# Performance work log

Measured on AMD Instinct MI355X. Metric: run time of the kernel, lower is better.

Reference implementation:

```python
import jax, jax.numpy as jnp
import numpy as np
import math

B, N, M = 4, 8192, 4096
POINT_DIM = 3
TIME_EMBED_DIM = 128
HIDDEN = (128, 256, 512, 512, 256)
EPS = 1e-5


def _silu(x):
    return x * jax.nn.sigmoid(x)


def _ln(x, g, b):
    m = x.mean(-1, keepdims=True)
    v = ((x - m) ** 2).mean(-1, keepdims=True)
    return (x - m) / jnp.sqrt(v + EPS) * g + b


def _blk(x, w, b, g, be):
    return _silu(_ln(x @ w + b, g, be))


def _linear_params(key, din, dout):
    return jax.random.normal(key, (din, dout), jnp.float32) * 0.02, jnp.zeros((dout,), jnp.float32)


def setup_inputs() -> dict:
    key = jax.random.key(0)
    ks = jax.random.split(key, 16)
    inp = {
        "noisy_points": jax.random.normal(ks[0], (B, N, POINT_DIM), jnp.float32),
        "target_points": jax.random.normal(ks[1], (B, M, POINT_DIM), jnp.float32),
        "timesteps": jax.random.uniform(ks[2], (B,), jnp.float32) * 1000.0,
    }
    # time embedding MLP: 128 -> 512 -> 512
    inp["te_w1"], inp["te_b1"] = _linear_params(ks[3], TIME_EMBED_DIM, TIME_EMBED_DIM * 4)
    inp["te_w2"], inp["te_b2"] = _linear_params(ks[4], TIME_EMBED_DIM * 4, TIME_EMBED_DIM * 4)
    # encoders: 6->128, 128->256, 256->512 (each Linear + LayerNorm)
    enc_dims = [(POINT_DIM * 2, HIDDEN[0]), (HIDDEN[0], HIDDEN[1]), (HIDDEN[1], HIDDEN[2])]
    for i, (di, do) in enumerate(enc_dims):
        inp[f"enc_w{i}"], inp[f"enc_b{i}"] = _linear_params(ks[5 + i], di, do)
        inp[f"enc_g{i}"] = jnp.ones((do,), jnp.float32)
        inp[f"enc_be{i}"] = jnp.zeros((do,), jnp.float32)
    # middle: (512 + 512) -> 512
    mid = HIDDEN[2]
    inp["mid_w"], inp["mid_b"] = _linear_params(ks[8], mid + TIME_EMBED_DIM * 4, mid)
    inp["mid_g"] = jnp.ones((mid,), jnp.float32)
    inp["mid_be"] = jnp.zeros((mid,), jnp.float32)
    # decoders: (512+256)->512, (512+128)->256
    dec_dims = [(mid + HIDDEN[1], HIDDEN[3]), (mid + HIDDEN[0], HIDDEN[4])]
    for i, (di, do) in enumerate(dec_dims):
        inp[f"dec_w{i}"], inp[f"dec_b{i}"] = _linear_params(ks[9 + i], di, do)
        inp[f"dec_g{i}"] = jnp.ones((do,), jnp.float32)
        inp[f"dec_be{i}"] = jnp.zeros((do,), jnp.float32)
    # output proj: 256 -> 3
    inp["out_w"], inp["out_b"] = _linear_params(ks[11], HIDDEN[4], POINT_DIM)
    return inp


def _time_embedding(timesteps, te_w1, te_b1, te_w2, te_b2):
    half = TIME_EMBED_DIM // 2
    freqs = jnp.exp(jnp.arange(half, dtype=jnp.float32) * (-math.log(10000.0) / (half - 1)))
    emb = timesteps[:, None] * freqs[None, :]  # (B, half)
    emb = jnp.concatenate([jnp.sin(emb), jnp.cos(emb)], axis=-1)  # (B, 128)
    return _silu(emb @ te_w1 + te_b1) @ te_w2 + te_b2  # (B, 512)


def _forward(noisy_points, target_points, timesteps,
             te_w1, te_b1, te_w2, te_b2,
             enc_w0, enc_b0, enc_g0, enc_be0,
             enc_w1, enc_b1, enc_g1, enc_be1,
             enc_w2, enc_b2, enc_g2, enc_be2,
             mid_w, mid_b, mid_g, mid_be,
             dec_w0, dec_b0, dec_g0, dec_be0,
             dec_w1, dec_b1, dec_g1, dec_be1,
             out_w, out_b):
    # nearest-neighbor lookup: squared distances share argmin with cdist
    d2 = (jnp.sum(noisy_points ** 2, -1)[:, :, None]
          + jnp.sum(target_points ** 2, -1)[:, None, :]
          - 2.0 * jnp.einsum('bnd,bmd->bnm', noisy_points, target_points))  # (B,N,M)
    idx = jnp.argmin(d2, axis=-1)  # (B,N)
    nearest = jnp.take_along_axis(
        target_points, jnp.broadcast_to(idx[:, :, None], idx.shape + (POINT_DIM,)), axis=1)
    x = jnp.concatenate([noisy_points, nearest], axis=-1)  # (B,N,6)
    skip0 = _blk(x, enc_w0, enc_b0, enc_g0, enc_be0)        # (B,N,128)
    skip1 = _blk(skip0, enc_w1, enc_b1, enc_g1, enc_be1)    # (B,N,256)
    x = _blk(skip1, enc_w2, enc_b2, enc_g2, enc_be2)        # (B,N,512)
    temb = _time_embedding(timesteps, te_w1, te_b1, te_w2, te_b2)  # (B,512)
    tfeat = jnp.broadcast_to(temb[:, None, :], (x.shape[0], x.shape[1], temb.shape[-1]))
    x = _blk(jnp.concatenate([x, tfeat], -1), mid_w, mid_b, mid_g, mid_be)      # (B,N,512)
    x = _blk(jnp.concatenate([x, skip1], -1), dec_w0, dec_b0, dec_g0, dec_be0)  # (B,N,512)
    x = _blk(jnp.concatenate([x, skip0], -1), dec_w1, dec_b1, dec_g1, dec_be1)  # (B,N,256)
    return x @ out_w + out_b  # (B,N,3)


def reference(noisy_points, target_points, timesteps,
              te_w1, te_b1, te_w2, te_b2,
              enc_w0, enc_b0, enc_g0, enc_be0,
              enc_w1, enc_b1, enc_g1, enc_be1,
              enc_w2, enc_b2, enc_g2, enc_be2,
              mid_w, mid_b, mid_g, mid_be,
              dec_w0, dec_b0, dec_g0, dec_be0,
              dec_w1, dec_b1, dec_g1, dec_be1,
              out_w, out_b):
    return _forward(noisy_points, target_points, timesteps,
                    te_w1, te_b1, te_w2, te_b2,
                    enc_w0, enc_b0, enc_g0, enc_be0,
                    enc_w1, enc_b1, enc_g1, enc_be1,
                    enc_w2, enc_b2, enc_g2, enc_be2,
                    mid_w, mid_b, mid_g, mid_be,
                    dec_w0, dec_b0, dec_g0, dec_be0,
                    dec_w1, dec_b1, dec_g1, dec_be1,
                    out_w, out_b)
```

## Files before the change

### kernel.cpp

```cpp
#include <hip/hip_runtime.h>
#include <stdint.h>

#define RTOT 32768
#define CR   16384
#define NPTS 8192
#define MPTS 4096
#define NCH 8
#define CHM 512

typedef float f4v __attribute__((ext_vector_type(4)));
typedef short s8v __attribute__((ext_vector_type(8)));

__device__ __forceinline__ float bq(float f) {
    union { float f; uint32_t i; } u; u.f = f;
    u.i = (u.i + 0x7FFFu + ((u.i >> 16) & 1u)) & 0xFFFF0000u;
    return u.f;
}
__device__ __forceinline__ unsigned short f2bfu(float f) {
    union { float f; uint32_t i; } u; u.f = f;
    return (unsigned short)((u.i + 0x7FFFu + ((u.i >> 16) & 1u)) >> 16);
}
__device__ __forceinline__ float bfu2f(unsigned short s) {
    union { uint32_t i; float f; } u; u.i = ((uint32_t)s) << 16;
    return u.f;
}

__global__ __launch_bounds__(256) void transpose_split_kernel(
    const float* __restrict__ W, unsigned short* __restrict__ Wth,
    unsigned short* __restrict__ Wtl, int K, int N) {
    int i = blockIdx.x * 256 + threadIdx.x;
    if (i < K * N) {
        int n = i / K;
        int k = i % K;
        float w = W[(size_t)k * N + n];
        unsigned short h = f2bfu(w);
        Wth[i] = h;
        Wtl[i] = f2bfu(w - bfu2f(h));
    }
}

__global__ __launch_bounds__(256) void te0_dual(
    const float* __restrict__ ts,
    const float* __restrict__ w1, const float* __restrict__ b1,
    float* __restrict__ e1, float* __restrict__ e1q) {
    const bool Qv = (blockIdx.z == 1);
    __shared__ float emb[128];
    const int b = blockIdx.y;
    const int j = blockIdx.x * 256 + threadIdx.x;
    float t = ts[b];
    if (threadIdx.x < 128) {
        int k = threadIdx.x & 63;
        float f = expf((float)k * -0.14619587892025688f);
        float a = t * f;
        float v = (threadIdx.x < 64) ? sinf(a) : cosf(a);
        emb[threadIdx.x] = Qv ? bq(v) : v;
    }
    __syncthreads();
    float acc = 0.f;
    #pragma unroll 8
    for (int k = 0; k < 128; k++) {
        float w = w1[(size_t)k * 512 + j];
        acc += emb[k] * (Qv ? bq(w) : w);
    }
    acc += b1[j];
    if (Qv) {
        float h = bq(acc);
        float sg = bq(1.f / (1.f + expf(-h)));
        e1q[b * 512 + j] = bq(h * sg);
    } else {
        e1[b * 512 + j] = acc / (1.f + expf(-acc));
    }
}

__global__ __launch_bounds__(256) void te1_dual(
    const float* __restrict__ e1, const float* __restrict__ e1q,
    const float* __restrict__ w2, const float* __restrict__ b2,
    unsigned short* __restrict__ tembh, unsigned short* __restrict__ tembl,
    unsigned short* __restrict__ tembq) {
    const bool Qv = (blockIdx.z == 1);
    __shared__ float es[512];
    const int b = blockIdx.y;
    const int j = blockIdx.x * 256 + threadIdx.x;
    const float* src = Qv ? e1q : e1;
    float v0 = src[b * 512 + threadIdx.x];
    float v1 = src[b * 512 + 256 + threadIdx.x];
    es[threadIdx.x] = Qv ? bq(v0) : v0;
    es[256 + threadIdx.x] = Qv ? bq(v1) : v1;
    __syncthreads();
    float acc = 0.f;
    #pragma unroll 8
    for (int k = 0; k < 512; k++) {
        float w = w2[(size_t)k * 512 + j];
        acc += es[k] * (Qv ? bq(w) : w);
    }
    acc += b2[j];
    if (Qv) {
        tembq[b * 512 + j] = f2bfu(acc);
    } else {
        unsigned short h = f2bfu(acc);
        tembh[b * 512 + j] = h;
        tembl[b * 512 + j] = f2bfu(acc - bfu2f(h));
    }
}

__global__ __launch_bounds__(256) void nn_partial_kernel(
    const float* __restrict__ NP, const float* __restrict__ TP,
    double* __restrict__ pd, int* __restrict__ pi) {
    __shared__ float tx[CHM], ty[CHM], tz[CHM];
    __shared__ double t264[CHM];
    const int t = threadIdx.x;
    const int r = blockIdx.x * 256 + t;
    const int b = r >> 13;
    const int ch = blockIdx.y;
    const int m0 = ch * CHM;
    for (int i = t; i < CHM; i += 256) {
        const float* p = TP + ((size_t)b * MPTS + m0 + i) * 3;
        float x = p[0], y = p[1], z = p[2];
        tx[i] = x; ty[i] = y; tz[i] = z;
        t264[i] = (double)x * x + (double)y * y + (double)z * z;
    }
    __syncthreads();
    const float* q = NP + (size_t)r * 3;
    double nx = (double)q[0], ny = (double)q[1], nz = (double)q[2];
    double sn = nx * nx + ny * ny + nz * nz;
    double g1 = 1e300; int j1 = 0;
    for (int m = 0; m < CHM; m++) {
        double d = (sn + t264[m]) - 2.0 * (nx * tx[m] + ny * ty[m] + nz * tz[m]);
        if (d < g1) { g1 = d; j1 = m; }
    }
    size_t o = (size_t)r * NCH + ch;
    pd[o] = g1;
    pi[o] = m0 + j1;
}

__global__ __launch_bounds__(256) void nn_merge_kernel(
    const float* __restrict__ NP, const float* __restrict__ TP,
    const double* __restrict__ pd, const int* __restrict__ pi,
    float* __restrict__ X0) {
    const int r = blockIdx.x * 256 + threadIdx.x;
    double g1 = 1e300; int j1 = 0;
    #pragma unroll
    for (int c = 0; c < NCH; c++) {
        size_t o = (size_t)r * NCH + c;
        double d = pd[o]; int i = pi[o];
        if (d < g1) { g1 = d; j1 = i; }
    }
    const int b = r >> 13;
    const float* tp = TP + ((size_t)b * MPTS + j1) * 3;
    const float* q = NP + (size_t)r * 3;
    float* o = X0 + (size_t)r * 6;
    o[0] = q[0]; o[1] = q[1]; o[2] = q[2];
    o[3] = tp[0]; o[4] = tp[1]; o[5] = tp[2];
}

__global__ __launch_bounds__(256) void layer0_dual(
    const float* __restrict__ X0, const float* __restrict__ W0,
    const float* __restrict__ b0, const float* __restrict__ g0,
    const float* __restrict__ e0,
    unsigned short* __restrict__ OutQ,
    unsigned short* __restrict__ OutFh, unsigned short* __restrict__ OutFl) {
    const bool Qp = (blockIdx.y == 0);
    const int wave = threadIdx.x >> 6;
    const int lane = threadIdx.x & 63;
    const int r = blockIdx.x * 4 + wave;
    float xk[6];
    #pragma unroll
    for (int k = 0; k < 6; k++) {
        float v = X0[(size_t)r * 6 + k];
        xk[k] = Qp ? bq(v) : v;
    }
    const int j0 = lane, j1 = lane + 64;
    float y0 = 0.f, y1 = 0.f;
    #pragma unroll
    for (int k = 0; k < 6; k++) {
        float w0 = W0[k * 128 + j0], w1 = W0[k * 128 + j1];
        y0 += xk[k] * (Qp ? bq(w0) : w0);
        y1 += xk[k] * (Qp ? bq(w1) : w1);
    }
    y0 += b0[j0];
    y1 += b0[j1];
    if (Qp) { y0 = bq(y0); y1 = bq(y1); }
    float s = y0 + y1;
    #pragma unroll
    for (int m = 1; m < 64; m <<= 1) s += __shfl_xor(s, m, 64);
    float mean = s * (1.f / 128.f);
    if (Qp) {
        mean = bq(mean);
        float c0 = bq(y0 - mean), c1 = bq(y1 - mean);
        float q0 = bq(c0 * c0), q1 = bq(c1 * c1);
        float sv = q0 + q1;
        #pragma unroll
        for (int m = 1; m < 64; m <<= 1) sv += __shfl_xor(sv, m, 64);
        float var = bq(sv * (1.f / 128.f));
        float sd = bq(sqrtf(bq(var + 1e-5f)));
        float d0 = bq(c0 / sd), d1 = bq(c1 / sd);
        d0 = bq(bq(d0 * g0[j0]) + e0[j0]);
        d1 = bq(bq(d1 * g0[j1]) + e0[j1]);
        float s0 = bq(1.f / (1.f + expf(-d0)));
        float s1 = bq(1.f / (1.f + expf(-d1)));
        OutQ[(size_t)r * 128 + j0] = f2bfu(d0 * s0);
        OutQ[(size_t)r * 128 + j1] = f2bfu(d1 * s1);
    } else {
        float sq = y0 * y0 + y1 * y1;
        #pragma unroll
        for (int m = 1; m < 64; m <<= 1) sq += __shfl_xor(sq, m, 64);
        float var = sq * (1.f / 128.f) - mean * mean;
        float rstd = rsqrtf(var + 1e-5f);
        float n0 = (y0 - mean) * rstd * g0[j0] + e0[j0];
        float n1 = (y1 - mean) * rstd * g0[j1] + e0[j1];
        float v0 = n0 / (1.f + expf(-n0));
        float v1 = n1 / (1.f + expf(-n1));
        unsigned short h0 = f2bfu(v0), h1 = f2bfu(v1);
        OutFh[(size_t)r * 128 + j0] = h0;
        OutFl[(size_t)r * 128 + j0] = f2bfu(v0 - bfu2f(h0));
        OutFh[(size_t)r * 128 + j1] = h1;
        OutFl[(size_t)r * 128 + j1] = f2bfu(v1 - bfu2f(h1));
    }
}

#define AP 72

template <int NOUT, bool FP>
__device__ __forceinline__ void mfma_body(
    const unsigned short* __restrict__ A1a, const unsigned short* __restrict__ A1b, int K1,
    const unsigned short* __restrict__ A2a, const unsigned short* __restrict__ A2b, int K2, int shift,
    const unsigned short* __restrict__ Wth,
    const unsigned short* __restrict__ Wtl,
    const float* __restrict__ bias,
    const float* __restrict__ gamma,
    const float* __restrict__ beta,
    unsigned short* __restrict__ OutQ,
    unsigned short* __restrict__ OutFh, unsigned short* __restrict__ OutFl,
    float* __restrict__ OutF32, int K,
    unsigned short* AhB, unsigned short* AlB, float (*lnS)[16], float (*lnQ)[16]) {
    constexpr int BNW = NOUT / 4;
    constexpr int CT = BNW / 16;
    constexpr int CHK = FP ? 2 : 4;

    const int tid = threadIdx.x;
    const int wave = tid >> 6;
    const int lane = tid & 63;
    const int q = lane >> 4;
    const int c = lane & 15;
    const int r0 = blockIdx.x * 64;
    const int trow = tid >> 2;
    const int tcol = (tid & 3) << 4;
    const int r = r0 + trow;

    f4v acc[4][CT];
    #pragma unroll
    for (int rt = 0; rt < 4; rt++)
        #pragma unroll
        for (int ct = 0; ct < CT; ct++)
            acc[rt][ct] = (f4v)0.f;

    s8v qa[2], qb[2];
    auto loadA = [&](int k0) {
        const int kk = k0 + tcol;
        const unsigned short *sa, *sb;
        size_t idx;
        if (k0 < K1) { sa = A1a; sb = A1b; idx = (size_t)r * K1 + kk; }
        else         { sa = A2a; sb = A2b; idx = (size_t)(r >> shift) * K2 + (kk - K1); }
        qa[0] = *(const s8v*)(sa + idx);
        qa[1] = *(const s8v*)(sa + idx + 8);
        if (FP) {
            qb[0] = *(const s8v*)(sb + idx);
            qb[1] = *(const s8v*)(sb + idx + 8);
        }
    };

    loadA(0);
    int cur = 0;
    for (int k0 = 0; k0 < K; k0 += 64) {
        unsigned short* Ah = AhB + cur * (64 * AP);
        unsigned short* Al = AlB + cur * (64 * AP);
        *(s8v*)(&Ah[trow * AP + tcol]) = qa[0];
        *(s8v*)(&Ah[trow * AP + tcol + 8]) = qa[1];
        if (FP) {
            *(s8v*)(&Al[trow * AP + tcol]) = qb[0];
            *(s8v*)(&Al[trow * AP + tcol + 8]) = qb[1];
        }
        if (k0 + 64 < K) loadA(k0 + 64);
        __syncthreads();
        __builtin_amdgcn_s_setprio(1);
        #pragma unroll
        for (int kh = 0; kh < 2; kh++) {
            const int kb = k0 + kh * 32;
            #pragma unroll
            for (int ctb = 0; ctb < CT; ctb += CHK) {
                s8v bh[CHK], bl[CHK];
                #pragma unroll
                for (int j = 0; j < CHK; j++) {
                    int col = wave * BNW + (ctb + j) * 16 + c;
                    bh[j] = *(const s8v*)(Wth + (size_t)col * K + kb + q * 8);
                    if (FP) bl[j] = *(const s8v*)(Wtl + (size_t)col * K + kb + q * 8);
                }
                #pragma unroll
                for (int rt = 0; rt < 4; rt++) {
                    s8v ah = *(const s8v*)(&Ah[(rt * 16 + c) * AP + kh * 32 + q * 8]);
                    if (FP) {
                        s8v al = *(const s8v*)(&Al[(rt * 16 + c) * AP + kh * 32 + q * 8]);
                        #pragma unroll
                        for (int j = 0; j < CHK; j++) {
                            acc[rt][ctb + j] = __builtin_amdgcn_mfma_f32_16x16x32_bf16(ah, bh[j], acc[rt][ctb + j], 0, 0, 0);
                            acc[rt][ctb + j] = __builtin_amdgcn_mfma_f32_16x16x32_bf16(ah, bl[j], acc[rt][ctb + j], 0, 0, 0);
                            acc[rt][ctb + j] = __builtin_amdgcn_mfma_f32_16x16x32_bf16(al, bh[j], acc[rt][ctb + j], 0, 0, 0);
                        }
                    } else {
                        #pragma unroll
                        for (int j = 0; j < CHK; j++)
                            acc[rt][ctb + j] = __builtin_amdgcn_mfma_f32_16x16x32_bf16(ah, bh[j], acc[rt][ctb + j], 0, 0, 0);
                    }
                }
            }
        }
        __builtin_amdgcn_s_setprio(0);
        cur ^= 1;
    }
    __syncthreads();

    float bcol[CT], gcol[CT], ecol[CT];
    #pragma unroll
    for (int ct = 0; ct < CT; ct++) {
        int col = wave * BNW + ct * 16 + c;
        bcol[ct] = bias[col];
        gcol[ct] = gamma[col];
        ecol[ct] = beta[col];
    }
    const float inv = 1.f / (float)NOUT;
    #pragma unroll
    for (int rt = 0; rt < 4; rt++) {
        if (FP) {
            float s[4] = {0.f, 0.f, 0.f, 0.f}, sq[4] = {0.f, 0.f, 0.f, 0.f};
            #pragma unroll
            for (int ct = 0; ct < CT; ct++)
                #pragma unroll
                for (int reg = 0; reg < 4; reg++) {
                    float v = acc[rt][ct][reg] + bcol[ct];
                    acc[rt][ct][reg] = v;
                    s[reg] += v;
                    sq[reg] += v * v;
                }
            #pragma unroll
            for (int m = 1; m < 16; m <<= 1)
                #pragma unroll
                for (int reg = 0; reg < 4; reg++) {
                    s[reg] += __shfl_xor(s[reg], m, 64);
                    sq[reg] += __shfl_xor(sq[reg], m, 64);
                }
            if (c == 0)
                #pragma unroll
                for (int reg = 0; reg < 4; reg++) {
                    lnS[wave][q * 4 + reg] = s[reg];
                    lnQ[wave][q * 4 + reg] = sq[reg];
                }
            __syncthreads();
            #pragma unroll
            for (int reg = 0; reg < 4; reg++) {
                int lr = q * 4 + reg;
                float S = lnS[0][lr] + lnS[1][lr] + lnS[2][lr] + lnS[3][lr];
                float SQ = lnQ[0][lr] + lnQ[1][lr] + lnQ[2][lr] + lnQ[3][lr];
                float mean = S * inv;
                float var = SQ * inv - mean * mean;
                float rstd = rsqrtf(var + 1e-5f);
                size_t rr = (size_t)(r0 + rt * 16 + lr);
                #pragma unroll
                for (int ct = 0; ct < CT; ct++) {
                    float y = (acc[rt][ct][reg] - mean) * rstd * gcol[ct] + ecol[ct];
                    float ys = y / (1.f + expf(-y));
                    size_t idx = rr * NOUT + wave * BNW + ct * 16 + c;
                    if (OutF32) {
                        OutF32[idx] = ys;
                    } else {
                        unsigned short h = f2bfu(ys);
                        OutFh[idx] = h;
                        OutFl[idx] = f2bfu(ys - bfu2f(h));
                    }
                }
            }
            __syncthreads();
        } else {
            float s[4] = {0.f, 0.f, 0.f, 0.f};
            #pragma unroll
            for (int ct = 0; ct < CT; ct++)
                #pragma unroll
                for (int reg = 0; reg < 4; reg++) {
                    float h = bq(acc[rt][ct][reg] + bcol[ct]);
                    acc[rt][ct][reg] = h;
                    s[reg] += h;
                }
            #pragma unroll
            for (int m = 1; m < 16; m <<= 1)
                #pragma unroll
                for (int reg = 0; reg < 4; reg++)
                    s[reg] += __shfl_xor(s[reg], m, 64);
            if (c == 0)
                #pragma unroll
                for (int reg = 0; reg < 4; reg++)
                    lnS[wave][q * 4 + reg] = s[reg];
            __syncthreads();
            float mean[4], sv[4] = {0.f, 0.f, 0.f, 0.f};
            #pragma unroll
            for (int reg = 0; reg < 4; reg++) {
                int lr = q * 4 + reg;
                mean[reg] = bq((lnS[0][lr] + lnS[1][lr] + lnS[2][lr] + lnS[3][lr]) * inv);
            }
            #pragma unroll
            for (int ct = 0; ct < CT; ct++)
                #pragma unroll
                for (int reg = 0; reg < 4; reg++) {
                    float cc = bq(acc[rt][ct][reg] - mean[reg]);
                    acc[rt][ct][reg] = cc;
                    sv[reg] += bq(cc * cc);
                }
            #pragma unroll
            for (int m = 1; m < 16; m <<= 1)
                #pragma unroll
                for (int reg = 0; reg < 4; reg++)
                    sv[reg] += __shfl_xor(sv[reg], m, 64);
            if (c == 0)
                #pragma unroll
                for (int reg = 0; reg < 4; reg++)
                    lnQ[wave][q * 4 + reg] = sv[reg];
            __syncthreads();
            #pragma unroll
            for (int reg = 0; reg < 4; reg++) {
                int lr = q * 4 + reg;
                float var = bq((lnQ[0][lr] + lnQ[1][lr] + lnQ[2][lr] + lnQ[3][lr]) * inv);
                float sd = bq(sqrtf(bq(var + 1e-5f)));
                size_t rr = (size_t)(r0 + rt * 16 + lr);
                #pragma unroll
                for (int ct = 0; ct < CT; ct++) {
                    float d = bq(acc[rt][ct][reg] / sd);
                    d = bq(bq(d * gcol[ct]) + ecol[ct]);
                    float sg = bq(1.f / (1.f + expf(-d)));
                    OutQ[rr * NOUT + wave * BNW + ct * 16 + c] = f2bfu(d * sg);
                }
            }
            __syncthreads();
        }
    }
}

template <int NOUT>
__global__ __launch_bounds__(256, 2) void mfma_dual(
    const unsigned short* __restrict__ A1q,
    const unsigned short* __restrict__ A1h, const unsigned short* __restrict__ A1l, int K1,
    const unsigned short* __restrict__ A2q,
    const unsigned short* __restrict__ A2h, const unsigned short* __restrict__ A2l, int K2, int shift,
    const unsigned short* __restrict__ Wth,
    const unsigned short* __restrict__ Wtl,
    const float* __restrict__ bias,
    const float* __restrict__ gamma,
    const float* __restrict__ beta,
    unsigned short* __restrict__ OutQ,
    unsigned short* __restrict__ OutFh, unsigned short* __restrict__ OutFl,
    float* __restrict__ OutF32, int K) {
    __shared__ unsigned short Ah[2][64 * AP];
    __shared__ unsigned short Al[2][64 * AP];
    __shared__ float lnS[4][16];
    __shared__ float lnQ[4][16];
    if (blockIdx.y == 0)
        mfma_body<NOUT, false>(A1q, nullptr, K1, A2q, nullptr, K2, shift, Wth, Wtl,
                               bias, gamma, beta, OutQ, nullptr, nullptr, nullptr, K,
                               &Ah[0][0], &Al[0][0], lnS, lnQ);
    else
        mfma_body<NOUT, true>(A1h, A1l, K1, A2h, A2l, K2, shift, Wth, Wtl,
                              bias, gamma, beta, OutQ, OutFh, OutFl, OutF32, K,
                              &Ah[0][0], &Al[0][0], lnS, lnQ);
}

__global__ __launch_bounds__(256) void outproj_fused(
    const unsigned short* __restrict__ Xq, const float* __restrict__ Xf,
    const float* __restrict__ W, const float* __restrict__ bO,
    float* __restrict__ Out) {
    const int wave = threadIdx.x >> 6;
    const int lane = threadIdx.x & 63;
    const int r = blockIdx.x * 4 + wave;
    float q0 = 0.f, q1 = 0.f, q2 = 0.f;
    float f0 = 0.f, f1 = 0.f, f2 = 0.f;
    #pragma unroll
    for (int i = 0; i < 4; i++) {
        int k = lane + i * 64;
        float xq = bfu2f(Xq[(size_t)r * 256 + k]);
        float xf = Xf[(size_t)r * 256 + k];
        float w0 = W[k * 3 + 0], w1 = W[k * 3 + 1], w2 = W[k * 3 + 2];
        q0 += xq * bq(w0); q1 += xq * bq(w1); q2 += xq * bq(w2);
        f0 += xf * w0;     f1 += xf * w1;     f2 += xf * w2;
    }
    #pragma unroll
    for (int m = 1; m < 64; m <<= 1) {
        q0 += __shfl_xor(q0, m, 64);
        q1 += __shfl_xor(q1, m, 64);
        q2 += __shfl_xor(q2, m, 64);
        f0 += __shfl_xor(f0, m, 64);
        f1 += __shfl_xor(f1, m, 64);
        f2 += __shfl_xor(f2, m, 64);
    }
    if (lane == 0) {
        float a0 = bq(q0 + bO[0]);
        float a1 = bq(q1 + bO[1]);
        float a2 = bq(q2 + bO[2]);
        Out[(size_t)r * 3 + 0] = 0.2f * (f0 + bO[0]) + 0.8f * a0;
        Out[(size_t)r * 3 + 1] = 0.2f * (f1 + bO[1]) + 0.8f * a1;
        Out[(size_t)r * 3 + 2] = 0.2f * (f2 + bO[2]) + 0.8f * a2;
    }
}

extern "C" void kernel_launch(void* const* d_in, const int* in_sizes, int n_in,
                              void* d_out, int out_size, void* d_ws, size_t ws_size,
                              hipStream_t stream) {
    (void)in_sizes; (void)n_in; (void)out_size; (void)ws_size;
    const float* noisy  = (const float*)d_in[0];
    const float* target = (const float*)d_in[1];
    const float* tsteps = (const float*)d_in[2];
    const float* te_w1  = (const float*)d_in[3];
    const float* te_b1  = (const float*)d_in[4];
    const float* te_w2  = (const float*)d_in[5];
    const float* te_b2  = (const float*)d_in[6];
    const float* enc_w0 = (const float*)d_in[7];
    const float* enc_b0 = (const float*)d_in[8];
    const float* enc_g0 = (const float*)d_in[9];
    const float* enc_e0 = (const float*)d_in[10];
    const float* enc_w1 = (const float*)d_in[11];
    const float* enc_b1 = (const float*)d_in[12];
    const float* enc_g1 = (const float*)d_in[13];
    const float* enc_e1 = (const float*)d_in[14];
    const float* enc_w2 = (const float*)d_in[15];
    const float* enc_b2 = (const float*)d_in[16];
    const float* enc_g2 = (const float*)d_in[17];
    const float* enc_e2 = (const float*)d_in[18];
    const float* mid_w  = (const float*)d_in[19];
    const float* mid_b  = (const float*)d_in[20];
    const float* mid_g  = (const float*)d_in[21];
    const float* mid_e  = (const float*)d_in[22];
    const float* dec_w0 = (const float*)d_in[23];
    const float* dec_b0 = (const float*)d_in[24];
    const float* dec_g0 = (const float*)d_in[25];
    const float* dec_e0 = (const float*)d_in[26];
    const float* dec_w1 = (const float*)d_in[27];
    const float* dec_b1 = (const float*)d_in[28];
    const float* dec_g1 = (const float*)d_in[29];
    const float* dec_e1 = (const float*)d_in[30];
    const float* out_w  = (const float*)d_in[31];
    const float* out_b  = (const float*)d_in[32];

    char* ws = (char*)d_ws;
    size_t off = 0;
    auto alloc = [&](size_t n) { char* p = ws + off; off += (n + 255) & ~(size_t)255; return p; };

    unsigned short* wt_enc1h = (unsigned short*)alloc((size_t)256 * 128 * 2);
    unsigned short* wt_enc1l = (unsigned short*)alloc((size_t)256 * 128 * 2);
    unsigned short* wt_enc2h = (unsigned short*)alloc((size_t)512 * 256 * 2);
    unsigned short* wt_enc2l = (unsigned short*)alloc((size_t)512 * 256 * 2);
    unsigned short* wt_midh  = (unsigned short*)alloc((size_t)512 * 1024 * 2);
    unsigned short* wt_midl  = (unsigned short*)alloc((size_t)512 * 1024 * 2);
    unsigned short* wt_dec0h = (unsigned short*)alloc((size_t)512 * 768 * 2);
    unsigned short* wt_dec0l = (unsigned short*)alloc((size_t)512 * 768 * 2);
    unsigned short* wt_dec1h = (unsigned short*)alloc((size_t)256 * 640 * 2);
    unsigned short* wt_dec1l = (unsigned short*)alloc((size_t)256 * 640 * 2);

    float* e1    = (float*)alloc((size_t)4 * 512 * 4);
    float* e1q   = (float*)alloc((size_t)4 * 512 * 4);
    unsigned short* tembh = (unsigned short*)alloc((size_t)4 * 512 * 2);
    unsigned short* tembl = (unsigned short*)alloc((size_t)4 * 512 * 2);
    unsigned short* tembq = (unsigned short*)alloc((size_t)4 * 512 * 2);
    float* x0    = (float*)alloc((size_t)RTOT * 6 * 4);

    unsigned short* skip0q  = (unsigned short*)alloc((size_t)CR * 128 * 2);
    unsigned short* skip1q  = (unsigned short*)alloc((size_t)CR * 256 * 2);
    unsigned short* xAq     = (unsigned short*)alloc((size_t)CR * 512 * 2);
    unsigned short* xBq     = (unsigned short*)alloc((size_t)CR * 512 * 2);
    unsigned short* skip0fh = (unsigned short*)alloc((size_t)CR * 128 * 2);
    unsigned short* skip0fl = (unsigned short*)alloc((size_t)CR * 128 * 2);
    unsigned short* skip1fh = (unsigned short*)alloc((size_t)CR * 256 * 2);
    unsigned short* skip1fl = (unsigned short*)alloc((size_t)CR * 256 * 2);
    unsigned short* xAfh    = (unsigned short*)alloc((size_t)CR * 512 * 2);
    unsigned short* xAfl    = (unsigned short*)alloc((size_t)CR * 512 * 2);
    unsigned short* xBfh    = (unsigned short*)alloc((size_t)CR * 512 * 2);
    unsigned short* xBfl    = (unsigned short*)alloc((size_t)CR * 512 * 2);
    float* xBf32 = (float*)alloc((size_t)CR * 512 * 4);

    const int NE = RTOT * NCH;
    double* pd = (double*)xBf32;
    int*    pi = (int*)(pd + NE);

    transpose_split_kernel<<<(256 * 128 + 255) / 256, 256, 0, stream>>>(enc_w1, wt_enc1h, wt_enc1l, 128, 256);
    transpose_split_kernel<<<(512 * 256 + 255) / 256, 256, 0, stream>>>(enc_w2, wt_enc2h, wt_enc2l, 256, 512);
    transpose_split_kernel<<<(512 * 1024 + 255) / 256, 256, 0, stream>>>(mid_w, wt_midh, wt_midl, 1024, 512);
    transpose_split_kernel<<<(512 * 768 + 255) / 256, 256, 0, stream>>>(dec_w0, wt_dec0h, wt_dec0l, 768, 512);
    transpose_split_kernel<<<(256 * 640 + 255) / 256, 256, 0, stream>>>(dec_w1, wt_dec1h, wt_dec1l, 640, 256);

    te0_dual<<<dim3(2, 4, 2), 256, 0, stream>>>(tsteps, te_w1, te_b1, e1, e1q);
    te1_dual<<<dim3(2, 4, 2), 256, 0, stream>>>(e1, e1q, te_w2, te_b2, tembh, tembl, tembq);

    nn_partial_kernel<<<dim3(128, NCH), 256, 0, stream>>>(noisy, target, pd, pi);
    nn_merge_kernel<<<128, 256, 0, stream>>>(noisy, target, pd, pi, x0);

    for (int ch = 0; ch < 2; ch++) {
        const float* x0c = x0 + (size_t)ch * CR * 6;
        const size_t to = (size_t)ch * 2 * 512;
        float* outc = (float*)d_out + (size_t)ch * CR * 3;

        layer0_dual<<<dim3(CR / 4, 2), 256, 0, stream>>>(
            x0c, enc_w0, enc_b0, enc_g0, enc_e0, skip0q, skip0fh, skip0fl);
        mfma_dual<256><<<dim3(CR / 64, 2), 256, 0, stream>>>(
            skip0q, skip0fh, skip0fl, 128, nullptr, nullptr, nullptr, 0, 0,
            wt_enc1h, wt_enc1l, enc_b1, enc_g1, enc_e1,
            skip1q, skip1fh, skip1fl, nullptr, 128);
        mfma_dual<512><<<dim3(CR / 64, 2), 256, 0, stream>>>(
            skip1q, skip1fh, skip1fl, 256, nullptr, nullptr, nullptr, 0, 0,
            wt_enc2h, wt_enc2l, enc_b2, enc_g2, enc_e2,
            xAq, xAfh, xAfl, nullptr, 256);
        mfma_dual<512><<<dim3(CR / 64, 2), 256, 0, stream>>>(
            xAq, xAfh, xAfl, 512, tembq + to, tembh + to, tembl + to, 512, 13,
            wt_midh, wt_midl, mid_b, mid_g, mid_e,
            xBq, xBfh, xBfl, nullptr, 1024);
        mfma_dual<512><<<dim3(CR / 64, 2), 256, 0, stream>>>(
            xBq, xBfh, xBfl, 512, skip1q, skip1fh, skip1fl, 256, 0,
            wt_dec0h, wt_dec0l, dec_b0, dec_g0, dec_e0,
            xAq, xAfh, xAfl, nullptr, 768);
        mfma_dual<256><<<dim3(CR / 64, 2), 256, 0, stream>>>(
            xAq, xAfh, xAfl, 512, skip0q, skip0fh, skip0fl, 128, 0,
            wt_dec1h, wt_dec1l, dec_b1, dec_g1, dec_e1,
            xBq, nullptr, nullptr, xBf32, 640);
        outproj_fused<<<CR / 4, 256, 0, stream>>>(xBq, xBf32, out_w, out_b, outc);
    }
}
```

Before: 1.086 ms.

## Stage A tiles via direct global-to-LDS loads with XOR-swizzled layout

```diff
diff --git a/kernel.cpp b/kernel.cpp
--- a/kernel.cpp
+++ b/kernel.cpp
@@ -10,6 +10,10 @@
 
 typedef float f4v __attribute__((ext_vector_type(4)));
 typedef short s8v __attribute__((ext_vector_type(8)));
+
+#define GLDS(src, dst) __builtin_amdgcn_global_load_lds( \
+    (const __attribute__((address_space(1))) void*)(const void*)(src), \
+    (__attribute__((address_space(3))) void*)(void*)(dst), 16, 0, 0)
 
 __device__ __forceinline__ float bq(float f) {
     union { float f; uint32_t i; } u; u.f = f;
@@ -218,8 +222,6 @@
     }
 }
 
-#define AP 72
-
 template <int NOUT, bool FP>
 __device__ __forceinline__ void mfma_body(
     const unsigned short* __restrict__ A1a, const unsigned short* __restrict__ A1b, int K1,
@@ -243,9 +245,6 @@
     const int q = lane >> 4;
     const int c = lane & 15;
     const int r0 = blockIdx.x * 64;
-    const int trow = tid >> 2;
-    const int tcol = (tid & 3) << 4;
-    const int r = r0 + trow;
 
     f4v acc[4][CT];
     #pragma unroll
@@ -254,34 +253,32 @@
         for (int ct = 0; ct < CT; ct++)
             acc[rt][ct] = (f4v)0.f;
 
-    s8v qa[2], qb[2];
-    auto loadA = [&](int k0) {
-        const int kk = k0 + tcol;
-        const unsigned short *sa, *sb;
-        size_t idx;
-        if (k0 < K1) { sa = A1a; sb = A1b; idx = (size_t)r * K1 + kk; }
-        else         { sa = A2a; sb = A2b; idx = (size_t)(r >> shift) * K2 + (kk - K1); }
-        qa[0] = *(const s8v*)(sa + idx);
-        qa[1] = *(const s8v*)(sa + idx + 8);
-        if (FP) {
-            qb[0] = *(const s8v*)(sb + idx);
-            qb[1] = *(const s8v*)(sb + idx + 8);
+    const int rofs = lane >> 3;
+    const int sslot = (lane & 7) ^ rofs;
+    auto stage = [&](int bufIdx, int k0) {
+        unsigned short* AhT = AhB + bufIdx * (64 * 64);
+        unsigned short* AlT = AlB + bufIdx * (64 * 64);
+        #pragma unroll
+        for (int half = 0; half < 2; half++) {
+            const int rowt = wave * 16 + half * 8 + rofs;
+            const int rg = r0 + rowt;
+            const unsigned short *sa, *sb;
+            size_t base;
+            if (k0 < K1) { sa = A1a; sb = A1b; base = (size_t)rg * K1 + k0; }
+            else         { sa = A2a; sb = A2b; base = (size_t)(rg >> shift) * K2 + (k0 - K1); }
+            GLDS(sa + base + sslot * 8, AhT + (wave * 16 + half * 8) * 64);
+            if (FP)
+                GLDS(sb + base + sslot * 8, AlT + (wave * 16 + half * 8) * 64);
         }
     };
 
-    loadA(0);
+    stage(0, 0);
+    __syncthreads();
     int cur = 0;
     for (int k0 = 0; k0 < K; k0 += 64) {
-        unsigned short* Ah = AhB + cur * (64 * AP);
-        unsigned short* Al = AlB + cur * (64 * AP);
-        *(s8v*)(&Ah[trow * AP + tcol]) = qa[0];
-        *(s8v*)(&Ah[trow * AP + tcol + 8]) = qa[1];
-        if (FP) {
-            *(s8v*)(&Al[trow * AP + tcol]) = qb[0];
-            *(s8v*)(&Al[trow * AP + tcol + 8]) = qb[1];
-        }
-        if (k0 + 64 < K) loadA(k0 + 64);
-        __syncthreads();
+        if (k0 + 64 < K) stage(cur ^ 1, k0 + 64);
+        unsigned short* Ah = AhB + cur * (64 * 64);
+        unsigned short* Al = AlB + cur * (64 * 64);
         __builtin_amdgcn_s_setprio(1);
         #pragma unroll
         for (int kh = 0; kh < 2; kh++) {
@@ -297,9 +294,10 @@
                 }
                 #pragma unroll
                 for (int rt = 0; rt < 4; rt++) {
-                    s8v ah = *(const s8v*)(&Ah[(rt * 16 + c) * AP + kh * 32 + q * 8]);
+                    const int koff = ((kh * 32 + q * 8) ^ ((c & 7) << 3));
+                    s8v ah = *(const s8v*)(&Ah[(rt * 16 + c) * 64 + koff]);
                     if (FP) {
-                        s8v al = *(const s8v*)(&Al[(rt * 16 + c) * AP + kh * 32 + q * 8]);
+                        s8v al = *(const s8v*)(&Al[(rt * 16 + c) * 64 + koff]);
                         #pragma unroll
                         for (int j = 0; j < CHK; j++) {
                             acc[rt][ctb + j] = __builtin_amdgcn_mfma_f32_16x16x32_bf16(ah, bh[j], acc[rt][ctb + j], 0, 0, 0);
@@ -315,9 +313,9 @@
             }
         }
         __builtin_amdgcn_s_setprio(0);
+        __syncthreads();
         cur ^= 1;
     }
-    __syncthreads();
 
     float bcol[CT], gcol[CT], ecol[CT];
     #pragma unroll
@@ -456,8 +454,8 @@
     unsigned short* __restrict__ OutQ,
     unsigned short* __restrict__ OutFh, unsigned short* __restrict__ OutFl,
     float* __restrict__ OutF32, int K) {
-    __shared__ unsigned short Ah[2][64 * AP];
-    __shared__ unsigned short Al[2][64 * AP];
+    __shared__ __align__(16) unsigned short Ah[2][64 * 64];
+    __shared__ __align__(16) unsigned short Al[2][64 * 64];
     __shared__ float lnS[4][16];
     __shared__ float lnQ[4][16];
     if (blockIdx.y == 0)
```

New measurement: 1.030 ms (median of 4 runs). 1.05x faster.
